# Optimization experiments

Hardware: AMD Instinct MI355X
Metric: run time of the kernel (lower is better)

The kernel has to match this reference:

```python
import jax, jax.numpy as jnp
import numpy as np
from jax import lax

DN = ('NCDHW', 'OIDHW', 'NCDHW')


def conv3(x, w, stride=1):
    return lax.conv_general_dilated(x, w, (stride,) * 3, 'VALID', dimension_numbers=DN)


def edge_pad(v):  # zero-gradient (Neumann) halo of width 1
    return jnp.pad(v, ((0, 0), (0, 0), (1, 1), (1, 1), (1, 1)), mode='edge')


def zero_pad(v):  # Dirichlet-0 halo for the MG correction
    return jnp.pad(v, ((0, 0), (0, 0), (1, 1), (1, 1), (1, 1)))


def bc_u(u, ub):  # Neumann everywhere, Dirichlet inlet (u=ub) on -x face
    p = edge_pad(u)
    return p.at[:, :, :, :, 0].set(jnp.asarray(ub, p.dtype))


def prol(x):  # nearest-neighbour upsample x2 (nn.Upsample scale_factor=2)
    for ax in (2, 3, 4):
        x = jnp.repeat(x, 2, axis=ax)
    return x


def setup_inputs() -> dict:
    N = 128
    key = jax.random.key(0)
    k = jax.random.split(key, 6)
    shp = (1, 1, N, N, N)
    # 7-point Laplacian stencil (A and diff)
    wA = np.zeros((1, 1, 3, 3, 3), np.float32)
    wA[0, 0, 1, 1, 1] = -6.0
    for d, h, w in [(0, 1, 1), (2, 1, 1), (1, 0, 1), (1, 2, 1), (1, 1, 0), (1, 1, 2)]:
        wA[0, 0, d, h, w] = 1.0
    w_diff = wA.copy()
    # central-difference advection stencils along W (x), H (y), D (z)
    w_xadv = np.zeros((1, 1, 3, 3, 3), np.float32)
    w_xadv[0, 0, 1, 1, 0], w_xadv[0, 0, 1, 1, 2] = -0.5, 0.5
    w_yadv = np.zeros((1, 1, 3, 3, 3), np.float32)
    w_yadv[0, 0, 1, 0, 1], w_yadv[0, 0, 1, 2, 1] = -0.5, 0.5
    w_zadv = np.zeros((1, 1, 3, 3, 3), np.float32)
    w_zadv[0, 0, 0, 1, 1], w_zadv[0, 0, 2, 1, 1] = -0.5, 0.5
    w_res = np.full((1, 1, 2, 2, 2), 0.125, np.float32)
    return {
        'values_u': jax.random.normal(k[0], shp, jnp.float32) * 0.1,
        'values_v': jax.random.normal(k[1], shp, jnp.float32) * 0.1,
        'values_w': jax.random.normal(k[2], shp, jnp.float32) * 0.1,
        'values_p': jax.random.normal(k[3], shp, jnp.float32) * 0.1,
        'sigma': jax.random.uniform(k[4], shp, jnp.float32) * 10.0,  # solid-body drag field
        'dt': jnp.asarray(0.05, jnp.float32),
        'wA': jnp.asarray(wA), 'w_diff': jnp.asarray(w_diff),
        'w_xadv': jnp.asarray(w_xadv), 'w_yadv': jnp.asarray(w_yadv),
        'w_zadv': jnp.asarray(w_zadv), 'w_res': jnp.asarray(w_res),
        'ub': 1, 'Re': 1, 'iteration': 2, 'nlevel': 9,
    }


def reference(values_u, values_v, values_w, values_p, sigma, dt,
              wA, w_diff, w_xadv, w_yadv, w_zadv, w_res,
              ub, Re, iteration, nlevel):
    diag = wA[0, 0, 1, 1, 1]
    A = lambda x: conv3(x, wA)
    diff = lambda x: conv3(x, w_diff)
    xadv = lambda x: conv3(x, w_xadv)
    yadv = lambda x: conv3(x, w_yadv)
    zadv = lambda x: conv3(x, w_zadv)
    res = lambda x: conv3(x, w_res, stride=2)

    def solid(u, v, w):
        f = 1.0 / (1.0 + dt * sigma)
        return u * f, v * f, w * f

    def pg(uu, vv, ww, u, v, w):  # Petrov-Galerkin dissipation (k fields == 1)
        one = jnp.ones_like(u)
        kp = edge_pad(one)
        ku = 0.5 * (one * diff(uu) + diff(uu * kp) - u * diff(kp))
        kv = 0.5 * (one * diff(vv) + diff(vv * kp) - v * diff(kp))
        kw = 0.5 * (one * diff(ww) + diff(ww * kp) - w * diff(kp))
        return ku, kv, kw

    u, v, w = solid(values_u, values_v, values_w)
    uu, vv, ww = bc_u(u, ub), edge_pad(v), edge_pad(w)
    pp = edge_pad(values_p)
    ku, kv, kw = pg(uu, vv, ww, u, v, w)
    # half-step predictor
    b_u = u + 0.5 * (Re * ku * dt - u * xadv(uu) * dt - v * yadv(uu) * dt - w * zadv(uu) * dt) - xadv(pp) * dt
    b_v = v + 0.5 * (Re * kv * dt - u * xadv(vv) * dt - v * yadv(vv) * dt - w * zadv(vv) * dt) - yadv(pp) * dt
    b_w = w + 0.5 * (Re * kw * dt - u * xadv(ww) * dt - v * yadv(ww) * dt - w * zadv(ww) * dt) - zadv(pp) * dt
    b_u, b_v, b_w = solid(b_u, b_v, b_w)
    buu, bvv, bww = bc_u(b_u, ub), edge_pad(b_v), edge_pad(b_w)
    ku, kv, kw = pg(buu, bvv, bww, b_u, b_v, b_w)
    # full-step corrector
    u = u + Re * ku * dt - b_u * xadv(buu) * dt - b_v * yadv(buu) * dt - b_w * zadv(buu) * dt - xadv(pp) * dt
    v = v + Re * kv * dt - b_u * xadv(bvv) * dt - b_v * yadv(bvv) * dt - b_w * zadv(bvv) * dt - yadv(pp) * dt
    w = w + Re * kw * dt - b_u * xadv(bww) * dt - b_v * yadv(bww) * dt - b_w * zadv(bww) * dt - zadv(pp) * dt
    u, v, w = solid(u, v, w)
    uu, vv, ww = bc_u(u, ub), edge_pad(v), edge_pad(w)
    # multigrid F-cycle pressure solve
    b = -(xadv(uu) + yadv(vv) + zadv(ww)) / dt
    p = values_p
    wmg = jnp.zeros((1, 1, 1, 1, 1), u.dtype)
    r = b
    for _ in range(iteration):
        wmg = jnp.zeros((1, 1, 1, 1, 1), u.dtype)
        r = A(pp) - b
        r_s = [r]
        for _i in range(1, nlevel - 1):
            r = res(r)
            r_s.append(r)
        for i in reversed(range(1, nlevel - 1)):
            wp = zero_pad(wmg)
            wmg = wmg - A(wp) / diag + r_s[i] / diag
            wmg = prol(wmg)
        p = p - wmg
        p = p - A(pp) / diag + b / diag
        pp = edge_pad(p)
    u = u - xadv(pp) * dt
    v = v - yadv(pp) * dt
    w = w - zadv(pp) * dt
    u, v, w = solid(u, v, w)
    return u, v, w, p, wmg, r
```

## Files before the change

kernel.cpp:

```cpp
#include <hip/hip_runtime.h>

#define NN 128
#define VV (NN*NN*NN)
#define GRID_MG 1024

typedef float v4 __attribute__((ext_vector_type(4)));
typedef unsigned short u16;

__device__ __forceinline__ float rcpf(float a){ return __builtin_amdgcn_rcpf(a); }
__device__ __forceinline__ v4 rcp4(v4 a){ v4 r; r.x=rcpf(a.x); r.y=rcpf(a.y); r.z=rcpf(a.z); r.w=rcpf(a.w); return r; }
__device__ __forceinline__ v4 mk4(float a,float b,float c,float d){ v4 r; r.x=a;r.y=b;r.z=c;r.w=d; return r; }
__device__ __forceinline__ int clampi(int a, int lo, int hi){ return min(max(a,lo),hi); }

__device__ __forceinline__ float b2f(u16 h){ union{unsigned u; float f;} c; c.u=((unsigned)h)<<16; return c.f; }
__device__ __forceinline__ u16 f2b(float f){
    union{float f; unsigned u;} c; c.f=f;
    unsigned rb = ((c.u>>16)&1u) + 0x7FFFu;
    return (u16)((c.u + rb)>>16);
}
__device__ __forceinline__ float ld1(const float* __restrict__ p, int o){ return p[o]; }
__device__ __forceinline__ float ld1(const u16*  __restrict__ p, int o){ return b2f(p[o]); }
__device__ __forceinline__ v4 ld4(const float* __restrict__ p, int o){ return *(const v4*)(p+o); }
__device__ __forceinline__ v4 ld4(const u16*  __restrict__ p, int o){
    ushort4 h = *(const ushort4*)(p+o);
    return mk4(b2f(h.x),b2f(h.y),b2f(h.z),b2f(h.w));
}
__device__ __forceinline__ void st4(float* __restrict__ p, int o, v4 v){ *(v4*)(p+o) = v; }
__device__ __forceinline__ void st4(u16*  __restrict__ p, int o, v4 v){
    ushort4 h; h.x=f2b(v.x); h.y=f2b(v.y); h.z=f2b(v.z); h.w=f2b(v.w);
    *(ushort4*)(p+o) = h;
}
template<typename T>
__device__ __forceinline__ float ldcT(const T* __restrict__ f, int z, int y, int x){
    z=clampi(z,0,NN-1); y=clampi(y,0,NN-1); x=clampi(x,0,NN-1);
    return ld1(f,(z*NN+y)*NN+x);
}

#define SETUP_OFFS \
    int i4 = (blockIdx.x*blockDim.x + threadIdx.x)<<2; \
    int x = i4 & 127, y = (i4>>7)&127, z = i4>>14; \
    bool x0 = (x==0), x1 = (x==124); \
    int o_c  = i4; \
    int o_ym = o_c + ((y>0)   ? -128   : 0); \
    int o_yp = o_c + ((y<127) ?  128   : 0); \
    int o_zm = o_c + ((z>0)   ? -16384 : 0); \
    int o_zp = o_c + ((z<127) ?  16384 : 0); \
    int o_xm = x0 ? o_c : o_c-1; \
    int o_xp = x1 ? o_c : o_c+4;

__global__ void __launch_bounds__(256) k_predict(
        const float* __restrict__ u_in, const float* __restrict__ v_in,
        const float* __restrict__ w_in, const float* __restrict__ p,
        const float* __restrict__ sg, const float* __restrict__ dtp,
        const int* __restrict__ ubp, const int* __restrict__ rep,
        u16* __restrict__ bu, u16* __restrict__ bv, u16* __restrict__ bw){
    SETUP_OFFS
    float dt = dtp[0], ub = (float)ubp[0], Re = (float)rep[0];
    float h = 0.5f*dt;

    v4 f_c  = rcp4(1.0f + dt*ld4(sg,o_c));
    v4 f_ym = rcp4(1.0f + dt*ld4(sg,o_ym));
    v4 f_yp = rcp4(1.0f + dt*ld4(sg,o_yp));
    v4 f_zm = rcp4(1.0f + dt*ld4(sg,o_zm));
    v4 f_zp = rcp4(1.0f + dt*ld4(sg,o_zp));
    float f_xm = rcpf(1.0f + dt*sg[o_xm]);
    float f_xp = rcpf(1.0f + dt*sg[o_xp]);

#define STEN(F, cen, vxm, vxp, vym, vyp, vzm, vzp, XMVAL) \
    v4 cen = ld4(F,o_c)*f_c; \
    v4 vym = ld4(F,o_ym)*f_ym; v4 vyp = ld4(F,o_yp)*f_yp; \
    v4 vzm = ld4(F,o_zm)*f_zm; v4 vzp = ld4(F,o_zp)*f_zp; \
    float cen##_xms = x0 ? (XMVAL) : F[o_xm]*f_xm; \
    float cen##_xps = x1 ? cen.w   : F[o_xp]*f_xp; \
    v4 vxm = mk4(cen##_xms, cen.x, cen.y, cen.z); \
    v4 vxp = mk4(cen.y, cen.z, cen.w, cen##_xps);

    STEN(u_in, uc, uxm, uxp, uym, uyp, uzm, uzp, ub)
    STEN(v_in, vc, vxm, vxp, vym, vyp, vzm, vzp, vc.x)
    STEN(w_in, wc, wxm, wxp, wym, wyp, wzm, wzp, wc.x)
#undef STEN

    v4 pc = ld4(p,o_c);
    v4 pym = ld4(p,o_ym), pyp = ld4(p,o_yp), pzm = ld4(p,o_zm), pzp = ld4(p,o_zp);
    float p_xms = x0 ? pc.x : p[o_xm];
    float p_xps = x1 ? pc.w : p[o_xp];
    v4 pxm = mk4(p_xms, pc.x, pc.y, pc.z);
    v4 pxp = mk4(pc.y, pc.z, pc.w, p_xps);
    v4 gpx = 0.5f*(pxp-pxm), gpy = 0.5f*(pyp-pym), gpz = 0.5f*(pzp-pzm);

    v4 lap_u = uxm+uxp+uym+uyp+uzm+uzp - 6.0f*uc;
    v4 lap_v = vxm+vxp+vym+vyp+vzm+vzp - 6.0f*vc;
    v4 lap_w = wxm+wxp+wym+wyp+wzm+wzp - 6.0f*wc;
    v4 xau=0.5f*(uxp-uxm), yau=0.5f*(uyp-uym), zau=0.5f*(uzp-uzm);
    v4 xav=0.5f*(vxp-vxm), yav=0.5f*(vyp-vym), zav=0.5f*(vzp-vzm);
    v4 xaw=0.5f*(wxp-wxm), yaw=0.5f*(wyp-wym), zaw=0.5f*(wzp-wzm);

    st4(bu,o_c, (uc + h*(Re*lap_u - (uc*xau + vc*yau + wc*zau)) - dt*gpx)*f_c);
    st4(bv,o_c, (vc + h*(Re*lap_v - (uc*xav + vc*yav + wc*zav)) - dt*gpy)*f_c);
    st4(bw,o_c, (wc + h*(Re*lap_w - (uc*xaw + vc*yaw + wc*zaw)) - dt*gpz)*f_c);
}

__global__ void __launch_bounds__(256) k_corr(
        const float* __restrict__ u_in, const float* __restrict__ v_in,
        const float* __restrict__ w_in,
        const u16* __restrict__ bu, const u16* __restrict__ bv,
        const u16* __restrict__ bw, const float* __restrict__ p,
        const float* __restrict__ sg, const float* __restrict__ dtp,
        const int* __restrict__ ubp, const int* __restrict__ rep,
        u16* __restrict__ ou, u16* __restrict__ ov, u16* __restrict__ ow){
    SETUP_OFFS
    float dt = dtp[0], ub = (float)ubp[0], Re = (float)rep[0];
    v4 f0 = rcp4(1.0f + dt*ld4(sg,o_c));
    v4 u0c = ld4(u_in,o_c)*f0, v0c = ld4(v_in,o_c)*f0, w0c = ld4(w_in,o_c)*f0;

#define STEN2(F, cen, vxm, vxp, vym, vyp, vzm, vzp, XMVAL) \
    v4 cen = ld4(F,o_c); \
    v4 vym = ld4(F,o_ym), vyp = ld4(F,o_yp), vzm = ld4(F,o_zm), vzp = ld4(F,o_zp); \
    float cen##_xms = x0 ? (XMVAL) : ld1(F,o_xm); \
    float cen##_xps = x1 ? cen.w   : ld1(F,o_xp); \
    v4 vxm = mk4(cen##_xms, cen.x, cen.y, cen.z); \
    v4 vxp = mk4(cen.y, cen.z, cen.w, cen##_xps);

    STEN2(bu, uc, uxm, uxp, uym, uyp, uzm, uzp, ub)
    STEN2(bv, vc, vxm, vxp, vym, vyp, vzm, vzp, vc.x)
    STEN2(bw, wc, wxm, wxp, wym, wyp, wzm, wzp, wc.x)
#undef STEN2

    v4 pc = ld4(p,o_c);
    v4 pym = ld4(p,o_ym), pyp = ld4(p,o_yp), pzm = ld4(p,o_zm), pzp = ld4(p,o_zp);
    float p_xms = x0 ? pc.x : p[o_xm];
    float p_xps = x1 ? pc.w : p[o_xp];
    v4 pxm = mk4(p_xms, pc.x, pc.y, pc.z);
    v4 pxp = mk4(pc.y, pc.z, pc.w, p_xps);
    v4 gpx = 0.5f*(pxp-pxm), gpy = 0.5f*(pyp-pym), gpz = 0.5f*(pzp-pzm);

    v4 lap_u = uxm+uxp+uym+uyp+uzm+uzp - 6.0f*uc;
    v4 lap_v = vxm+vxp+vym+vyp+vzm+vzp - 6.0f*vc;
    v4 lap_w = wxm+wxp+wym+wyp+wzm+wzp - 6.0f*wc;
    v4 xau=0.5f*(uxp-uxm), yau=0.5f*(uyp-uym), zau=0.5f*(uzp-uzm);
    v4 xav=0.5f*(vxp-vxm), yav=0.5f*(vyp-vym), zav=0.5f*(vzp-vzm);
    v4 xaw=0.5f*(wxp-wxm), yaw=0.5f*(wyp-wym), zaw=0.5f*(wzp-wzm);

    st4(ou,o_c, (u0c + dt*(Re*lap_u - (uc*xau + vc*yau + wc*zau)) - dt*gpx)*f0);
    st4(ov,o_c, (v0c + dt*(Re*lap_v - (uc*xav + vc*yav + wc*zav)) - dt*gpy)*f0);
    st4(ow,o_c, (w0c + dt*(Re*lap_w - (uc*xaw + vc*yaw + wc*zaw)) - dt*gpz)*f0);
}

__device__ __forceinline__ float j1_eval(const float* __restrict__ r1, const float* __restrict__ j2,
                                         int X, int Y, int Z){
    float s = 0.f;
    s += (X>0 ) ? j2[((Z>>1)*32+(Y>>1))*32+((X-1)>>1)] : 0.f;
    s += (X<63) ? j2[((Z>>1)*32+(Y>>1))*32+((X+1)>>1)] : 0.f;
    s += (Y>0 ) ? j2[((Z>>1)*32+((Y-1)>>1))*32+(X>>1)] : 0.f;
    s += (Y<63) ? j2[((Z>>1)*32+((Y+1)>>1))*32+(X>>1)] : 0.f;
    s += (Z>0 ) ? j2[(((Z-1)>>1)*32+(Y>>1))*32+(X>>1)] : 0.f;
    s += (Z<63) ? j2[(((Z+1)>>1)*32+(Y>>1))*32+(X>>1)] : 0.f;
    return (s - r1[(Z*64+Y)*64+X]) * (1.0f/6.0f);
}

__device__ void chain_restrict(const float* __restrict__ src, float* __restrict__ dst,
                               int nd, int t, int nt){
    int nd3 = nd*nd*nd, ns = nd*2;
    for (int c = t; c < nd3; c += nt){
        int X = c % nd, Y = (c/nd) % nd, Z = c/(nd*nd);
        float a = 0.f;
        for (int dz=0;dz<2;++dz)
          for (int dy=0;dy<2;++dy)
            for (int dx=0;dx<2;++dx)
                a += src[((2*Z+dz)*ns + (2*Y+dy))*ns + (2*X+dx)];
        dst[c] = 0.125f*a;
    }
}
__device__ void chain_jacobi(const float* jin, const float* r,
                             float* jout, int n, int t, int nt){
    int n3 = n*n*n, hn = n>>1;
    for (int c = t; c < n3; c += nt){
        int X = c % n, Y = (c/n) % n, Z = c/(n*n);
        float s = 0.f;
        s += (X>0  ) ? jin[((Z>>1)*hn+(Y>>1))*hn+((X-1)>>1)] : 0.f;
        s += (X<n-1) ? jin[((Z>>1)*hn+(Y>>1))*hn+((X+1)>>1)] : 0.f;
        s += (Y>0  ) ? jin[((Z>>1)*hn+((Y-1)>>1))*hn+(X>>1)] : 0.f;
        s += (Y<n-1) ? jin[((Z>>1)*hn+((Y+1)>>1))*hn+(X>>1)] : 0.f;
        s += (Z>0  ) ? jin[(((Z-1)>>1)*hn+(Y>>1))*hn+(X>>1)] : 0.f;
        s += (Z<n-1) ? jin[(((Z+1)>>1)*hn+(Y>>1))*hn+(X>>1)] : 0.f;
        jout[c] = (s - r[c]) * (1.0f/6.0f);
    }
}

__global__ void __launch_bounds__(1024) k_chain(
        const float* __restrict__ r3g, const float* __restrict__ r2g,
        float* __restrict__ j2, float* __restrict__ r7){
    __shared__ float r3[4096], r4[512], r5[64], r6[8], j7[1];
    int t = threadIdx.x; const int nt = 1024;
    for (int c = t; c < 4096; c += nt) r3[c] = r3g[c];
    __syncthreads();
    chain_restrict(r3, r4,  8, t, nt); __syncthreads();
    chain_restrict(r4, r5,  4, t, nt); __syncthreads();
    chain_restrict(r5, r6,  2, t, nt); __syncthreads();
    if (t == 0){
        float a = 0.f;
        for (int k=0;k<8;++k) a += r6[k];
        float rv = 0.125f*a;
        r7[0] = rv;
        j7[0] = -rv*(1.0f/6.0f);
    }
    __syncthreads();
    chain_jacobi(j7, r6, r6,  2, t, nt); __syncthreads();
    chain_jacobi(r6, r5, r5,  4, t, nt); __syncthreads();
    chain_jacobi(r5, r4, r4,  8, t, nt); __syncthreads();
    chain_jacobi(r4, r3, r3, 16, t, nt); __syncthreads();
    for (int c = t; c < 32*32*32; c += nt){
        int X = c & 31, Y = (c>>5)&31, Z = c>>10;
        float s = 0.f;
        s += (X>0 ) ? r3[((Z>>1)*16+(Y>>1))*16+((X-1)>>1)] : 0.f;
        s += (X<31) ? r3[((Z>>1)*16+(Y>>1))*16+((X+1)>>1)] : 0.f;
        s += (Y>0 ) ? r3[((Z>>1)*16+((Y-1)>>1))*16+(X>>1)] : 0.f;
        s += (Y<31) ? r3[((Z>>1)*16+((Y+1)>>1))*16+(X>>1)] : 0.f;
        s += (Z>0 ) ? r3[(((Z-1)>>1)*16+(Y>>1))*16+(X>>1)] : 0.f;
        s += (Z<31) ? r3[(((Z+1)>>1)*16+(Y>>1))*16+(X>>1)] : 0.f;
        j2[c] = (s - r2g[c]) * (1.0f/6.0f);
    }
}

__global__ void __launch_bounds__(512) k_mg1(
        const u16* __restrict__ u, const u16* __restrict__ v, const u16* __restrict__ w,
        const float* __restrict__ p, const float* __restrict__ dtp,
        const int* __restrict__ ubp,
        u16* __restrict__ b, float* __restrict__ r1, float* __restrict__ r2g,
        float* __restrict__ r3g){
    __shared__ float b_s[16*16*8];
    __shared__ float ph[512];
    __shared__ float r1_s[256];
    __shared__ float r2_s[32];
    int t = threadIdx.x;
    int BX = blockIdx.x & 7, BY = (blockIdx.x>>3)&7, BZ = blockIdx.x>>6;
    float dt = dtp[0], ub = (float)ubp[0];
    float rdt = rcpf(dt);

    {
        int tx4 = t & 3, fy = (t>>2)&15, fz = t>>6;
        int gx = BX*16 + tx4*4, gy = BY*16 + fy, gz = BZ*8 + fz;
        int o_c = (gz*NN+gy)*NN + gx;
        bool x0 = (gx==0), x1 = (gx==124);
        int o_ym = o_c + ((gy>0)    ? -NN    : 0);
        int o_yp = o_c + ((gy<NN-1) ?  NN    : 0);
        int o_zm = o_c + ((gz>0)    ? -NN*NN : 0);
        int o_zp = o_c + ((gz<NN-1) ?  NN*NN : 0);
        int o_xm = x0 ? o_c : o_c-1, o_xp = x1 ? o_c : o_c+4;
        v4 ucv = ld4(u,o_c);
        float u_xms = x0 ? ub    : ld1(u,o_xm);
        float u_xps = x1 ? ucv.w : ld1(u,o_xp);
        v4 uxm = mk4(u_xms, ucv.x, ucv.y, ucv.z);
        v4 uxp = mk4(ucv.y, ucv.z, ucv.w, u_xps);
        v4 vym = ld4(v,o_ym), vyp = ld4(v,o_yp);
        v4 wzm = ld4(w,o_zm), wzp = ld4(w,o_zp);
        v4 db = -(0.5f*((uxp-uxm)+(vyp-vym)+(wzp-wzm)))*rdt;
        st4(b,o_c,db);
        *(v4*)&b_s[(fz*16+fy)*16 + tx4*4] = db;
    }
    __syncthreads();
    {
        int cc = t & 255, h = t >> 8;
        int CX = cc&7, CY = (cc>>3)&7, CZ = cc>>6;
        int GX = BX*8+CX, GY = BY*8+CY, GZ = BZ*4+CZ;
        int z = 2*GZ+h;
        float acc = 0.f;
        #pragma unroll
        for (int dy=0;dy<2;++dy)
        #pragma unroll
        for (int dx=0;dx<2;++dx){
            int y = 2*GY+dy, x = 2*GX+dx;
            float pc = p[(z*NN+y)*NN+x];
            float lap = ldcT(p,z,y,x-1)+ldcT(p,z,y,x+1)+ldcT(p,z,y-1,x)+ldcT(p,z,y+1,x)
                      + ldcT(p,z-1,y,x)+ldcT(p,z+1,y,x) - 6.0f*pc;
            acc += lap - b_s[((2*CZ+h)*16+(2*CY+dy))*16+(2*CX+dx)];
        }
        ph[t] = acc;
    }
    __syncthreads();
    if (t < 256){
        int CX = t&7, CY = (t>>3)&7, CZ = t>>6;
        int GX = BX*8+CX, GY = BY*8+CY, GZ = BZ*4+CZ;
        float rv = 0.125f*(ph[t] + ph[t+256]);
        r1[(GZ*64+GY)*64+GX] = rv;
        r1_s[t] = rv;
    }
    __syncthreads();
    if (t < 32){
        int X = t&3, Y = (t>>2)&3, Z = t>>4;
        float a = 0.f;
        #pragma unroll
        for (int dz=0;dz<2;++dz)
        #pragma unroll
        for (int dy=0;dy<2;++dy)
        #pragma unroll
        for (int dx=0;dx<2;++dx)
            a += r1_s[((2*Z+dz)*8+(2*Y+dy))*8+(2*X+dx)];
        float r2v = 0.125f*a;
        r2g[((BZ*2+Z)*32 + (BY*4+Y))*32 + (BX*4+X)] = r2v;
        r2_s[t] = r2v;
    }
    __syncthreads();
    if (t < 4){
        int X2 = t&1, Y2 = t>>1;
        float a = 0.f;
        #pragma unroll
        for (int dz=0;dz<2;++dz)
        #pragma unroll
        for (int dy=0;dy<2;++dy)
        #pragma unroll
        for (int dx=0;dx<2;++dx)
            a += r2_s[dz*16 + (2*Y2+dy)*4 + (2*X2+dx)];
        r3g[(BZ*16 + (BY*2+Y2))*16 + (BX*2+X2)] = 0.125f*a;
    }
}

template<typename PT>
__global__ void __launch_bounds__(256) k_pupd(
        const PT* __restrict__ p, const float* __restrict__ r1,
        const float* __restrict__ j2, const u16* __restrict__ b,
        u16* __restrict__ pout){
    SETUP_OFFS
    v4 pc = ld4(p,o_c);
    v4 pym = ld4(p,o_ym), pyp = ld4(p,o_yp), pzm = ld4(p,o_zm), pzp = ld4(p,o_zp);
    float p_xms = x0 ? pc.x : ld1(p,o_xm);
    float p_xps = x1 ? pc.w : ld1(p,o_xp);
    v4 pxm = mk4(p_xms, pc.x, pc.y, pc.z);
    v4 pxp = mk4(pc.y, pc.z, pc.w, p_xps);
    v4 lap = pxm+pxp+pym+pyp+pzm+pzp - 6.0f*pc;
    v4 b4 = ld4(b,o_c);
    float j1a = j1_eval(r1, j2, (x>>1),   y>>1, z>>1);
    float j1b = j1_eval(r1, j2, (x>>1)+1, y>>1, z>>1);
    v4 j1v = mk4(j1a, j1a, j1b, j1b);
    st4(pout,o_c, pc - j1v + (lap - b4)*(1.0f/6.0f));
}

__global__ void __launch_bounds__(512) k_rr2f(
        const u16* __restrict__ P1, const u16* __restrict__ b,
        float* __restrict__ r1b, float* __restrict__ r2g, float* __restrict__ r3g){
    __shared__ float res_s[16*16*8];
    __shared__ float r1_s[256];
    __shared__ float r2_s[32];
    int t = threadIdx.x;
    int BX = blockIdx.x & 7, BY = (blockIdx.x>>3)&7, BZ = blockIdx.x>>6;

    {
        int tx4 = t & 3, fy = (t>>2)&15, fz = t>>6;
        int gx = BX*16 + tx4*4, gy = BY*16 + fy, gz = BZ*8 + fz;
        int o_c = (gz*NN+gy)*NN + gx;
        bool x0 = (gx==0), x1 = (gx==124);
        int o_ym = o_c + ((gy>0)    ? -NN    : 0);
        int o_yp = o_c + ((gy<NN-1) ?  NN    : 0);
        int o_zm = o_c + ((gz>0)    ? -NN*NN : 0);
        int o_zp = o_c + ((gz<NN-1) ?  NN*NN : 0);
        int o_xm = x0 ? o_c : o_c-1, o_xp = x1 ? o_c : o_c+4;
        v4 pc = ld4(P1,o_c);
        v4 pym = ld4(P1,o_ym), pyp = ld4(P1,o_yp), pzm = ld4(P1,o_zm), pzp = ld4(P1,o_zp);
        float p_xms = x0 ? pc.x : ld1(P1,o_xm);
        float p_xps = x1 ? pc.w : ld1(P1,o_xp);
        v4 pxm = mk4(p_xms, pc.x, pc.y, pc.z);
        v4 pxp = mk4(pc.y, pc.z, pc.w, p_xps);
        v4 res = pxm+pxp+pym+pyp+pzm+pzp - 6.0f*pc - ld4(b,o_c);
        *(v4*)&res_s[(fz*16+fy)*16 + tx4*4] = res;
    }
    __syncthreads();
    if (t < 256){
        int CX = t&7, CY = (t>>3)&7, CZ = t>>6;
        int GX = BX*8+CX, GY = BY*8+CY, GZ = BZ*4+CZ;
        float a = 0.f;
        #pragma unroll
        for (int dz=0;dz<2;++dz)
        #pragma unroll
        for (int dy=0;dy<2;++dy)
        #pragma unroll
        for (int dx=0;dx<2;++dx)
            a += res_s[((2*CZ+dz)*16+(2*CY+dy))*16+(2*CX+dx)];
        float rv = 0.125f*a;
        r1b[(GZ*64+GY)*64+GX] = rv;
        r1_s[t] = rv;
    }
    __syncthreads();
    if (t < 32){
        int X = t&3, Y = (t>>2)&3, Z = t>>4;
        float a = 0.f;
        #pragma unroll
        for (int dz=0;dz<2;++dz)
        #pragma unroll
        for (int dy=0;dy<2;++dy)
        #pragma unroll
        for (int dx=0;dx<2;++dx)
            a += r1_s[((2*Z+dz)*8+(2*Y+dy))*8+(2*X+dx)];
        float r2v = 0.125f*a;
        r2g[((BZ*2+Z)*32 + (BY*4+Y))*32 + (BX*4+X)] = r2v;
        r2_s[t] = r2v;
    }
    __syncthreads();
    if (t < 4){
        int X2 = t&1, Y2 = t>>1;
        float a = 0.f;
        #pragma unroll
        for (int dz=0;dz<2;++dz)
        #pragma unroll
        for (int dy=0;dy<2;++dy)
        #pragma unroll
        for (int dx=0;dx<2;++dx)
            a += r2_s[dz*16 + (2*Y2+dy)*4 + (2*X2+dx)];
        r3g[(BZ*16 + (BY*2+Y2))*16 + (BX*2+X2)] = 0.125f*a;
    }
}

__global__ void __launch_bounds__(256) k_final(
        const u16* __restrict__ u, const u16* __restrict__ v,
        const u16* __restrict__ w, const u16* __restrict__ p,
        const float* __restrict__ r1, const float* __restrict__ j2,
        const float* __restrict__ r7, const float* __restrict__ sg,
        const float* __restrict__ dtp, float* __restrict__ out){
    SETUP_OFFS
    float dt = dtp[0];
    v4 pc = ld4(p,o_c);
    v4 pym = ld4(p,o_ym), pyp = ld4(p,o_yp), pzm = ld4(p,o_zm), pzp = ld4(p,o_zp);
    float p_xms = x0 ? pc.x : ld1(p,o_xm);
    float p_xps = x1 ? pc.w : ld1(p,o_xp);
    v4 pxm = mk4(p_xms, pc.x, pc.y, pc.z);
    v4 pxp = mk4(pc.y, pc.z, pc.w, p_xps);
    v4 gpx = 0.5f*(pxp-pxm), gpy = 0.5f*(pyp-pym), gpz = 0.5f*(pzp-pzm);
    v4 f0 = rcp4(1.0f + dt*ld4(sg,o_c));
    st4(out, o_c,                        (ld4(u,o_c) - dt*gpx)*f0);
    st4(out + (size_t)VV, o_c,           (ld4(v,o_c) - dt*gpy)*f0);
    st4(out + 2*(size_t)VV, o_c,         (ld4(w,o_c) - dt*gpz)*f0);
    st4(out + 3*(size_t)VV, o_c,         pc);
    float j1a = j1_eval(r1, j2, (x>>1),   y>>1, z>>1);
    float j1b = j1_eval(r1, j2, (x>>1)+1, y>>1, z>>1);
    st4(out + 4*(size_t)VV, o_c,         mk4(j1a, j1a, j1b, j1b));
    if (i4 == 0) out[5*(size_t)VV] = r7[0];
}

extern "C" void kernel_launch(void* const* d_in, const int* in_sizes, int n_in,
                              void* d_out, int out_size, void* d_ws, size_t ws_size,
                              hipStream_t stream){
    (void)in_sizes; (void)n_in; (void)out_size; (void)ws_size;
    const float* u_in = (const float*)d_in[0];
    const float* v_in = (const float*)d_in[1];
    const float* w_in = (const float*)d_in[2];
    const float* p_in = (const float*)d_in[3];
    const float* sg   = (const float*)d_in[4];
    const float* dtp  = (const float*)d_in[5];
    const int*  ubp   = (const int*)d_in[12];
    const int*  rep   = (const int*)d_in[13];

    u16* wh = (u16*)d_ws;
    const size_t V = VV;
    u16* bu = wh;
    u16* bv = wh +   V;
    u16* bw = wh + 2*V;
    u16* u  = wh + 3*V;
    u16* v  = wh + 4*V;
    u16* w  = wh + 5*V;
    u16* b  = wh + 6*V;
    u16* P1 = wh + 7*V;
    u16* P2 = wh + 8*V;
    float* fs  = (float*)(wh + 10*V);
    float* r1a = fs;
    float* r1b = r1a + 64*64*64;
    float* r2  = r1b + 64*64*64;
    float* j2  = r2  + 32*32*32;
    float* r3g = j2  + 32*32*32;
    float* r7  = r3g + 16*16*16;

    dim3 blk(256);
    int g4 = (VV/4)/256;

    k_predict<<<g4, blk, 0, stream>>>(u_in,v_in,w_in,p_in,sg,dtp,ubp,rep,bu,bv,bw);
    k_corr   <<<g4, blk, 0, stream>>>(u_in,v_in,w_in,bu,bv,bw,p_in,sg,dtp,ubp,rep,u,v,w);
    k_mg1  <<<GRID_MG, 512, 0, stream>>>(u,v,w,p_in,dtp,ubp,b,r1a,r2,r3g);
    k_chain<<<1, 1024, 0, stream>>>(r3g, r2, j2, r7);
    k_pupd<float><<<g4, blk, 0, stream>>>(p_in, r1a, j2, b, P1);
    k_rr2f <<<GRID_MG, 512, 0, stream>>>(P1, b, r1b, r2, r3g);
    k_chain<<<1, 1024, 0, stream>>>(r3g, r2, j2, r7);
    k_pupd<u16><<<g4, blk, 0, stream>>>(P1, r1b, j2, b, P2);
    k_final<<<g4, blk, 0, stream>>>(u,v,w,P2,r1b,j2,r7,sg,dtp,(float*)d_out);
}
```

Measured before the change: 231.6 us.

## Precompute level-1 MG correction once per cycle and restructure stencil register usage

```diff
diff --git a/kernel.cpp b/kernel.cpp
--- a/kernel.cpp
+++ b/kernel.cpp
@@ -29,11 +29,6 @@
 __device__ __forceinline__ void st4(u16*  __restrict__ p, int o, v4 v){
     ushort4 h; h.x=f2b(v.x); h.y=f2b(v.y); h.z=f2b(v.z); h.w=f2b(v.w);
     *(ushort4*)(p+o) = h;
-}
-template<typename T>
-__device__ __forceinline__ float ldcT(const T* __restrict__ f, int z, int y, int x){
-    z=clampi(z,0,NN-1); y=clampi(y,0,NN-1); x=clampi(x,0,NN-1);
-    return ld1(f,(z*NN+y)*NN+x);
 }
 
 #define SETUP_OFFS \
@@ -66,19 +61,9 @@
     float f_xm = rcpf(1.0f + dt*sg[o_xm]);
     float f_xp = rcpf(1.0f + dt*sg[o_xp]);
 
-#define STEN(F, cen, vxm, vxp, vym, vyp, vzm, vzp, XMVAL) \
-    v4 cen = ld4(F,o_c)*f_c; \
-    v4 vym = ld4(F,o_ym)*f_ym; v4 vyp = ld4(F,o_yp)*f_yp; \
-    v4 vzm = ld4(F,o_zm)*f_zm; v4 vzp = ld4(F,o_zp)*f_zp; \
-    float cen##_xms = x0 ? (XMVAL) : F[o_xm]*f_xm; \
-    float cen##_xps = x1 ? cen.w   : F[o_xp]*f_xp; \
-    v4 vxm = mk4(cen##_xms, cen.x, cen.y, cen.z); \
-    v4 vxp = mk4(cen.y, cen.z, cen.w, cen##_xps);
-
-    STEN(u_in, uc, uxm, uxp, uym, uyp, uzm, uzp, ub)
-    STEN(v_in, vc, vxm, vxp, vym, vyp, vzm, vzp, vc.x)
-    STEN(w_in, wc, wxm, wxp, wym, wyp, wzm, wzp, wc.x)
-#undef STEN
+    v4 uc = ld4(u_in,o_c)*f_c;
+    v4 vc = ld4(v_in,o_c)*f_c;
+    v4 wc = ld4(w_in,o_c)*f_c;
 
     v4 pc = ld4(p,o_c);
     v4 pym = ld4(p,o_ym), pyp = ld4(p,o_yp), pzm = ld4(p,o_zm), pzp = ld4(p,o_zp);
@@ -88,16 +73,21 @@
     v4 pxp = mk4(pc.y, pc.z, pc.w, p_xps);
     v4 gpx = 0.5f*(pxp-pxm), gpy = 0.5f*(pyp-pym), gpz = 0.5f*(pzp-pzm);
 
-    v4 lap_u = uxm+uxp+uym+uyp+uzm+uzp - 6.0f*uc;
-    v4 lap_v = vxm+vxp+vym+vyp+vzm+vzp - 6.0f*vc;
-    v4 lap_w = wxm+wxp+wym+wyp+wzm+wzp - 6.0f*wc;
-    v4 xau=0.5f*(uxp-uxm), yau=0.5f*(uyp-uym), zau=0.5f*(uzp-uzm);
-    v4 xav=0.5f*(vxp-vxm), yav=0.5f*(vyp-vym), zav=0.5f*(vzp-vzm);
-    v4 xaw=0.5f*(wxp-wxm), yaw=0.5f*(wyp-wym), zaw=0.5f*(wzp-wzm);
-
-    st4(bu,o_c, (uc + h*(Re*lap_u - (uc*xau + vc*yau + wc*zau)) - dt*gpx)*f_c);
-    st4(bv,o_c, (vc + h*(Re*lap_v - (uc*xav + vc*yav + wc*zav)) - dt*gpy)*f_c);
-    st4(bw,o_c, (wc + h*(Re*lap_w - (uc*xaw + vc*yaw + wc*zaw)) - dt*gpz)*f_c);
+#define FIELD(F, cen, XMVAL, OUT, GP) { \
+    v4 vym = ld4(F,o_ym)*f_ym; v4 vyp = ld4(F,o_yp)*f_yp; \
+    v4 vzm = ld4(F,o_zm)*f_zm; v4 vzp = ld4(F,o_zp)*f_zp; \
+    float xms = x0 ? (XMVAL) : F[o_xm]*f_xm; \
+    float xps = x1 ? cen.w   : F[o_xp]*f_xp; \
+    v4 vxm = mk4(xms, cen.x, cen.y, cen.z); \
+    v4 vxp = mk4(cen.y, cen.z, cen.w, xps); \
+    v4 lap = vxm+vxp+vym+vyp+vzm+vzp - 6.0f*cen; \
+    v4 xa = 0.5f*(vxp-vxm), ya = 0.5f*(vyp-vym), za = 0.5f*(vzp-vzm); \
+    st4(OUT,o_c, (cen + h*(Re*lap - (uc*xa + vc*ya + wc*za)) - dt*(GP))*f_c); }
+
+    FIELD(u_in, uc, ub,   bu, gpx)
+    FIELD(v_in, vc, vc.x, bv, gpy)
+    FIELD(w_in, wc, wc.x, bw, gpz)
+#undef FIELD
 }
 
 __global__ void __launch_bounds__(256) k_corr(
@@ -112,19 +102,7 @@
     float dt = dtp[0], ub = (float)ubp[0], Re = (float)rep[0];
     v4 f0 = rcp4(1.0f + dt*ld4(sg,o_c));
     v4 u0c = ld4(u_in,o_c)*f0, v0c = ld4(v_in,o_c)*f0, w0c = ld4(w_in,o_c)*f0;
-
-#define STEN2(F, cen, vxm, vxp, vym, vyp, vzm, vzp, XMVAL) \
-    v4 cen = ld4(F,o_c); \
-    v4 vym = ld4(F,o_ym), vyp = ld4(F,o_yp), vzm = ld4(F,o_zm), vzp = ld4(F,o_zp); \
-    float cen##_xms = x0 ? (XMVAL) : ld1(F,o_xm); \
-    float cen##_xps = x1 ? cen.w   : ld1(F,o_xp); \
-    v4 vxm = mk4(cen##_xms, cen.x, cen.y, cen.z); \
-    v4 vxp = mk4(cen.y, cen.z, cen.w, cen##_xps);
-
-    STEN2(bu, uc, uxm, uxp, uym, uyp, uzm, uzp, ub)
-    STEN2(bv, vc, vxm, vxp, vym, vyp, vzm, vzp, vc.x)
-    STEN2(bw, wc, wxm, wxp, wym, wyp, wzm, wzp, wc.x)
-#undef STEN2
+    v4 uc = ld4(bu,o_c), vc = ld4(bv,o_c), wcv = ld4(bw,o_c);
 
     v4 pc = ld4(p,o_c);
     v4 pym = ld4(p,o_ym), pyp = ld4(p,o_yp), pzm = ld4(p,o_zm), pzp = ld4(p,o_zp);
@@ -134,16 +112,20 @@
     v4 pxp = mk4(pc.y, pc.z, pc.w, p_xps);
     v4 gpx = 0.5f*(pxp-pxm), gpy = 0.5f*(pyp-pym), gpz = 0.5f*(pzp-pzm);
 
-    v4 lap_u = uxm+uxp+uym+uyp+uzm+uzp - 6.0f*uc;
-    v4 lap_v = vxm+vxp+vym+vyp+vzm+vzp - 6.0f*vc;
-    v4 lap_w = wxm+wxp+wym+wyp+wzm+wzp - 6.0f*wc;
-    v4 xau=0.5f*(uxp-uxm), yau=0.5f*(uyp-uym), zau=0.5f*(uzp-uzm);
-    v4 xav=0.5f*(vxp-vxm), yav=0.5f*(vyp-vym), zav=0.5f*(vzp-vzm);
-    v4 xaw=0.5f*(wxp-wxm), yaw=0.5f*(wyp-wym), zaw=0.5f*(wzp-wzm);
-
-    st4(ou,o_c, (u0c + dt*(Re*lap_u - (uc*xau + vc*yau + wc*zau)) - dt*gpx)*f0);
-    st4(ov,o_c, (v0c + dt*(Re*lap_v - (uc*xav + vc*yav + wc*zav)) - dt*gpy)*f0);
-    st4(ow,o_c, (w0c + dt*(Re*lap_w - (uc*xaw + vc*yaw + wc*zaw)) - dt*gpz)*f0);
+#define FIELD2(F, cen, XMVAL, U0, OUT, GP) { \
+    v4 vym = ld4(F,o_ym), vyp = ld4(F,o_yp), vzm = ld4(F,o_zm), vzp = ld4(F,o_zp); \
+    float xms = x0 ? (XMVAL) : ld1(F,o_xm); \
+    float xps = x1 ? cen.w   : ld1(F,o_xp); \
+    v4 vxm = mk4(xms, cen.x, cen.y, cen.z); \
+    v4 vxp = mk4(cen.y, cen.z, cen.w, xps); \
+    v4 lap = vxm+vxp+vym+vyp+vzm+vzp - 6.0f*cen; \
+    v4 xa = 0.5f*(vxp-vxm), ya = 0.5f*(vyp-vym), za = 0.5f*(vzp-vzm); \
+    st4(OUT,o_c, (U0 + dt*(Re*lap - (uc*xa + vc*ya + wcv*za)) - dt*(GP))*f0); }
+
+    FIELD2(bu, uc,  ub,    u0c, ou, gpx)
+    FIELD2(bv, vc,  vc.x,  v0c, ov, gpy)
+    FIELD2(bw, wcv, wcv.x, w0c, ow, gpz)
+#undef FIELD2
 }
 
 __device__ __forceinline__ float j1_eval(const float* __restrict__ r1, const float* __restrict__ j2,
@@ -222,14 +204,26 @@
     }
 }
 
+__global__ void __launch_bounds__(256) k_j1(
+        const float* __restrict__ r1, const float* __restrict__ j2,
+        float* __restrict__ wmg){
+    int i4 = (blockIdx.x*blockDim.x + threadIdx.x)<<2;
+    int X = i4 & 63, Y = (i4>>6)&63, Z = i4>>12;
+    v4 o;
+    o.x = j1_eval(r1, j2, X,   Y, Z);
+    o.y = j1_eval(r1, j2, X+1, Y, Z);
+    o.z = j1_eval(r1, j2, X+2, Y, Z);
+    o.w = j1_eval(r1, j2, X+3, Y, Z);
+    st4(wmg, i4, o);
+}
+
 __global__ void __launch_bounds__(512) k_mg1(
         const u16* __restrict__ u, const u16* __restrict__ v, const u16* __restrict__ w,
         const float* __restrict__ p, const float* __restrict__ dtp,
         const int* __restrict__ ubp,
         u16* __restrict__ b, float* __restrict__ r1, float* __restrict__ r2g,
         float* __restrict__ r3g){
-    __shared__ float b_s[16*16*8];
-    __shared__ float ph[512];
+    __shared__ float res_s[16*16*8];
     __shared__ float r1_s[256];
     __shared__ float r2_s[32];
     int t = threadIdx.x;
@@ -256,32 +250,28 @@
         v4 wzm = ld4(w,o_zm), wzp = ld4(w,o_zp);
         v4 db = -(0.5f*((uxp-uxm)+(vyp-vym)+(wzp-wzm)))*rdt;
         st4(b,o_c,db);
-        *(v4*)&b_s[(fz*16+fy)*16 + tx4*4] = db;
-    }
-    __syncthreads();
-    {
-        int cc = t & 255, h = t >> 8;
-        int CX = cc&7, CY = (cc>>3)&7, CZ = cc>>6;
-        int GX = BX*8+CX, GY = BY*8+CY, GZ = BZ*4+CZ;
-        int z = 2*GZ+h;
-        float acc = 0.f;
-        #pragma unroll
-        for (int dy=0;dy<2;++dy)
-        #pragma unroll
-        for (int dx=0;dx<2;++dx){
-            int y = 2*GY+dy, x = 2*GX+dx;
-            float pc = p[(z*NN+y)*NN+x];
-            float lap = ldcT(p,z,y,x-1)+ldcT(p,z,y,x+1)+ldcT(p,z,y-1,x)+ldcT(p,z,y+1,x)
-                      + ldcT(p,z-1,y,x)+ldcT(p,z+1,y,x) - 6.0f*pc;
-            acc += lap - b_s[((2*CZ+h)*16+(2*CY+dy))*16+(2*CX+dx)];
-        }
-        ph[t] = acc;
+        v4 pc = ld4(p,o_c);
+        v4 pym = ld4(p,o_ym), pyp = ld4(p,o_yp), pzm = ld4(p,o_zm), pzp = ld4(p,o_zp);
+        float p_xms = x0 ? pc.x : p[o_xm];
+        float p_xps = x1 ? pc.w : p[o_xp];
+        v4 pxm = mk4(p_xms, pc.x, pc.y, pc.z);
+        v4 pxp = mk4(pc.y, pc.z, pc.w, p_xps);
+        v4 res = pxm+pxp+pym+pyp+pzm+pzp - 6.0f*pc - db;
+        *(v4*)&res_s[(fz*16+fy)*16 + tx4*4] = res;
     }
     __syncthreads();
     if (t < 256){
         int CX = t&7, CY = (t>>3)&7, CZ = t>>6;
         int GX = BX*8+CX, GY = BY*8+CY, GZ = BZ*4+CZ;
-        float rv = 0.125f*(ph[t] + ph[t+256]);
+        float a = 0.f;
+        #pragma unroll
+        for (int dz=0;dz<2;++dz)
+        #pragma unroll
+        for (int dy=0;dy<2;++dy)
+        #pragma unroll
+        for (int dx=0;dx<2;++dx)
+            a += res_s[((2*CZ+dz)*16+(2*CY+dy))*16+(2*CX+dx)];
+        float rv = 0.125f*a;
         r1[(GZ*64+GY)*64+GX] = rv;
         r1_s[t] = rv;
     }
@@ -317,9 +307,8 @@
 
 template<typename PT>
 __global__ void __launch_bounds__(256) k_pupd(
-        const PT* __restrict__ p, const float* __restrict__ r1,
-        const float* __restrict__ j2, const u16* __restrict__ b,
-        u16* __restrict__ pout){
+        const PT* __restrict__ p, const float* __restrict__ wmg,
+        const u16* __restrict__ b, u16* __restrict__ pout){
     SETUP_OFFS
     v4 pc = ld4(p,o_c);
     v4 pym = ld4(p,o_ym), pyp = ld4(p,o_yp), pzm = ld4(p,o_zm), pzp = ld4(p,o_zp);
@@ -329,9 +318,8 @@
     v4 pxp = mk4(pc.y, pc.z, pc.w, p_xps);
     v4 lap = pxm+pxp+pym+pyp+pzm+pzp - 6.0f*pc;
     v4 b4 = ld4(b,o_c);
-    float j1a = j1_eval(r1, j2, (x>>1),   y>>1, z>>1);
-    float j1b = j1_eval(r1, j2, (x>>1)+1, y>>1, z>>1);
-    v4 j1v = mk4(j1a, j1a, j1b, j1b);
+    const float2 jp = *(const float2*)(wmg + ((z>>1)*64 + (y>>1))*64 + (x>>1));
+    v4 j1v = mk4(jp.x, jp.x, jp.y, jp.y);
     st4(pout,o_c, pc - j1v + (lap - b4)*(1.0f/6.0f));
 }
 
@@ -412,9 +400,9 @@
 __global__ void __launch_bounds__(256) k_final(
         const u16* __restrict__ u, const u16* __restrict__ v,
         const u16* __restrict__ w, const u16* __restrict__ p,
-        const float* __restrict__ r1, const float* __restrict__ j2,
-        const float* __restrict__ r7, const float* __restrict__ sg,
-        const float* __restrict__ dtp, float* __restrict__ out){
+        const float* __restrict__ wmg, const float* __restrict__ r7,
+        const float* __restrict__ sg, const float* __restrict__ dtp,
+        float* __restrict__ out){
     SETUP_OFFS
     float dt = dtp[0];
     v4 pc = ld4(p,o_c);
@@ -429,9 +417,8 @@
     st4(out + (size_t)VV, o_c,           (ld4(v,o_c) - dt*gpy)*f0);
     st4(out + 2*(size_t)VV, o_c,         (ld4(w,o_c) - dt*gpz)*f0);
     st4(out + 3*(size_t)VV, o_c,         pc);
-    float j1a = j1_eval(r1, j2, (x>>1),   y>>1, z>>1);
-    float j1b = j1_eval(r1, j2, (x>>1)+1, y>>1, z>>1);
-    st4(out + 4*(size_t)VV, o_c,         mk4(j1a, j1a, j1b, j1b));
+    const float2 jp = *(const float2*)(wmg + ((z>>1)*64 + (y>>1))*64 + (x>>1));
+    st4(out + 4*(size_t)VV, o_c,         mk4(jp.x, jp.x, jp.y, jp.y));
     if (i4 == 0) out[5*(size_t)VV] = r7[0];
 }
 
@@ -460,23 +447,25 @@
     u16* P1 = wh + 7*V;
     u16* P2 = wh + 8*V;
     float* fs  = (float*)(wh + 10*V);
-    float* r1a = fs;
-    float* r1b = r1a + 64*64*64;
-    float* r2  = r1b + 64*64*64;
+    float* r1  = fs;
+    float* r2  = r1  + 64*64*64;
     float* j2  = r2  + 32*32*32;
     float* r3g = j2  + 32*32*32;
-    float* r7  = r3g + 16*16*16;
+    float* wmg = r3g + 16*16*16;
+    float* r7  = wmg + 64*64*64;
 
     dim3 blk(256);
     int g4 = (VV/4)/256;
 
     k_predict<<<g4, blk, 0, stream>>>(u_in,v_in,w_in,p_in,sg,dtp,ubp,rep,bu,bv,bw);
     k_corr   <<<g4, blk, 0, stream>>>(u_in,v_in,w_in,bu,bv,bw,p_in,sg,dtp,ubp,rep,u,v,w);
-    k_mg1  <<<GRID_MG, 512, 0, stream>>>(u,v,w,p_in,dtp,ubp,b,r1a,r2,r3g);
+    k_mg1  <<<GRID_MG, 512, 0, stream>>>(u,v,w,p_in,dtp,ubp,b,r1,r2,r3g);
     k_chain<<<1, 1024, 0, stream>>>(r3g, r2, j2, r7);
-    k_pupd<float><<<g4, blk, 0, stream>>>(p_in, r1a, j2, b, P1);
-    k_rr2f <<<GRID_MG, 512, 0, stream>>>(P1, b, r1b, r2, r3g);
+    k_j1   <<<256, blk, 0, stream>>>(r1, j2, wmg);
+    k_pupd<float><<<g4, blk, 0, stream>>>(p_in, wmg, b, P1);
+    k_rr2f <<<GRID_MG, 512, 0, stream>>>(P1, b, r1, r2, r3g);
     k_chain<<<1, 1024, 0, stream>>>(r3g, r2, j2, r7);
-    k_pupd<u16><<<g4, blk, 0, stream>>>(P1, r1b, j2, b, P2);
-    k_final<<<g4, blk, 0, stream>>>(u,v,w,P2,r1b,j2,r7,sg,dtp,(float*)d_out);
-}
+    k_j1   <<<256, blk, 0, stream>>>(r1, j2, wmg);
+    k_pupd<u16><<<g4, blk, 0, stream>>>(P1, wmg, b, P2);
+    k_final<<<g4, blk, 0, stream>>>(u,v,w,P2,wmg,r7,sg,dtp,(float*)d_out);
+}
```

Result: no change. 231.1 us (-0.2%).
